# Kernel optimization log

Hardware: AMD Instinct MI355X
Metric: run time of the kernel (lower is better)

Reference implementation:

```python
import jax, jax.numpy as jnp
import numpy as np

L = 2    # num_graph_layers
T = 16   # num_tasks (batch of episodes)
N = 128  # num_samples (nodes per episode)
F = 128  # num_node_feats
BN_EPS = 1e-5


def setup_inputs() -> dict:
    key = jax.random.key(0)
    ks = jax.random.split(key, 8)
    return {
        "node_feats": jax.random.normal(ks[0], (T, N, F), dtype=jnp.float32),
        "edge_feats": jax.random.uniform(ks[1], (T, N, N, F), dtype=jnp.float32),
        # Conv3d(3->1, 1x1x1) weight+bias per layer -> 3 scalars + 1 bias
        "edge_w": (jax.random.normal(ks[2], (L, 3), dtype=jnp.float32) * 0.5),
        "edge_b": (jax.random.normal(ks[3], (L,), dtype=jnp.float32) * 0.1),
        # Conv2d(2->1, 1x1, no bias) -> 2 scalars per layer
        "comb_w": (jax.random.normal(ks[4], (L, 2), dtype=jnp.float32) * 0.5),
        # Conv1d(F->F, k=1, no bias) -> [out,in] per layer
        "node_w": (jax.random.normal(ks[5], (L, F, F), dtype=jnp.float32) / np.sqrt(F).astype(np.float32)),
        # BatchNorm1d affine params
        "bn_gamma": jnp.ones((L, F), dtype=jnp.float32),
        "bn_beta": jnp.zeros((L, F), dtype=jnp.float32),
    }


def _lrelu(x):
    return jnp.where(x >= 0, x, 0.01 * x)  # torch LeakyReLU default slope


def _sim_cal(x):
    # x: [T,N,F] -> clamped [cos_sim, 1-cos_sim]: [T,2,N,N]
    g = jnp.einsum('tnf,tmf->tnm', x, x)
    nrm = jnp.linalg.norm(x, axis=-1)              # [T,N]
    denom = nrm[:, :, None] * nrm[:, None, :] + 1e-6
    sim = (g / denom)[:, None]                     # [T,1,N,N]
    pred = jnp.concatenate([sim, 1.0 - sim], axis=1)
    return jnp.clip(pred, 0.0, 1.0)


def reference(node_feats, edge_feats, edge_w, edge_b, comb_w, node_w, bn_gamma, bn_beta):
    outs = [_sim_cal(node_feats)]
    n = node_feats.shape[1]
    diag_mask = (1.0 - jnp.eye(n, dtype=node_feats.dtype))[None, :, :, None]  # [1,N,N,1]
    for l in range(L):
        x = node_feats                                     # [T,N,F]
        # --- EdgeUpdateNetwork: Conv3d(3->1,1x1x1) over channels [x_i, x_i-x_j, edge] + tanh ---
        diff = x[:, :, None, :] - x[:, None, :, :]         # [T,N,N,F]
        xi = jnp.broadcast_to(x[:, :, None, :], diff.shape)
        e = jnp.tanh(edge_w[l, 0] * xi + edge_w[l, 1] * diff
                     + edge_w[l, 2] * edge_feats + edge_b[l])
        edge_feats = e * diag_mask                         # zero diagonal
        # --- NodeUpdateNetwork ---
        aggr = edge_feats.sum(axis=2)                      # [T,N,F]
        h = _lrelu(comb_w[l, 0] * x + comb_w[l, 1] * aggr) # Conv2d(2->1) + LeakyReLU
        y = jnp.einsum('tnf,gf->tng', h, node_w[l])        # Conv1d(F->F, k=1)
        mu = y.mean(axis=(0, 1))                           # BN over (batch, length)
        var = y.var(axis=(0, 1))
        y = (y - mu) * jax.lax.rsqrt(var + BN_EPS) * bn_gamma[l] + bn_beta[l]
        node_feats = _lrelu(y)
        outs.append(_sim_cal(node_feats))
    return tuple(outs)
```

## Files before the change

kernel.cpp:

```cpp
#include <hip/hip_runtime.h>

#define T_ 16
#define N_ 128
#define F_ 128

__device__ __forceinline__ float fast_tanh(float x) {
    float e = __expf(2.0f * x);
    return 1.0f - __fdividef(2.0f, e + 1.0f);
}

__device__ __forceinline__ float lrelu(float v) {
    return v >= 0.0f ? v : 0.01f * v;
}

__global__ __launch_bounds__(128) void sim_cal_k(const float* __restrict__ x,
                                                 float* __restrict__ out) {
    __shared__ float Xs[128][132];
    __shared__ float nrm[128];
    int t = blockIdx.x, ch = blockIdx.y;
    int m = threadIdx.x;
    const float* xt = x + (size_t)t * (N_ * F_);

    int fg = (m & 31) * 4, ko = m >> 5;
    for (int kb = 0; kb < 128; kb += 4) {
        int k = kb + ko;
        float4 v = *(const float4*)(xt + k * 128 + fg);
        *(float4*)&Xs[k][fg] = v;
    }
    __syncthreads();

    float s = 0.0f;
    #pragma unroll 8
    for (int f = 0; f < 128; f += 4) {
        float4 v = *(float4*)&Xs[m][f];
        s += v.x * v.x + v.y * v.y + v.z * v.z + v.w * v.w;
    }
    nrm[m] = sqrtf(s);
    __syncthreads();

    float acc[16];
    #pragma unroll
    for (int r = 0; r < 16; ++r) acc[r] = 0.0f;

    for (int fc = 0; fc < 128; fc += 32) {
        float xm[32];
        #pragma unroll
        for (int f = 0; f < 32; f += 4) {
            float4 v = *(float4*)&Xs[m][fc + f];
            xm[f] = v.x; xm[f + 1] = v.y; xm[f + 2] = v.z; xm[f + 3] = v.w;
        }
        #pragma unroll
        for (int r = 0; r < 16; ++r) {
            int n = ch * 16 + r;
            #pragma unroll
            for (int f = 0; f < 32; f += 4) {
                float4 v = *(float4*)&Xs[n][fc + f];
                acc[r] = fmaf(xm[f], v.x,
                         fmaf(xm[f + 1], v.y,
                         fmaf(xm[f + 2], v.z,
                         fmaf(xm[f + 3], v.w, acc[r]))));
            }
        }
    }

    float nm = nrm[m];
    size_t ob = (size_t)t * 2 * 16384;
    #pragma unroll
    for (int r = 0; r < 16; ++r) {
        int n = ch * 16 + r;
        float denom = nrm[n] * nm + 1e-6f;
        float sim = __fdividef(acc[r], denom);
        float s0 = fminf(fmaxf(sim, 0.0f), 1.0f);
        float s1 = fminf(fmaxf(1.0f - sim, 0.0f), 1.0f);
        out[ob + (size_t)n * 128 + m] = s0;
        out[ob + 16384 + (size_t)n * 128 + m] = s1;
    }
}

__global__ __launch_bounds__(128) void edge_aggr_l0(const float* __restrict__ x0,
                                                    const float* __restrict__ E,
                                                    const float* __restrict__ ew,
                                                    const float* __restrict__ eb,
                                                    float* __restrict__ aggr) {
    int ti = blockIdx.x;
    int t = ti >> 7, i = ti & 127;
    int tid = threadIdx.x;
    int jl = tid >> 5, fg = tid & 31;
    float w0 = ew[0], w1 = ew[1], w2 = ew[2], b = eb[0];
    const float4* xt = (const float4*)(x0 + (size_t)t * 16384);
    const float4* Ei = (const float4*)(E + (size_t)ti * 16384);
    float4 xi = xt[i * 32 + fg];
    float ax = 0.0f, ay = 0.0f, az = 0.0f, aw = 0.0f;
    #pragma unroll 4
    for (int jb = 0; jb < 128; jb += 4) {
        int j = jb + jl;
        float4 xj = xt[j * 32 + fg];
        float4 ev = Ei[j * 32 + fg];
        if (j != i) {
            ax += fast_tanh(fmaf(w0, xi.x, fmaf(w1, xi.x - xj.x, fmaf(w2, ev.x, b))));
            ay += fast_tanh(fmaf(w0, xi.y, fmaf(w1, xi.y - xj.y, fmaf(w2, ev.y, b))));
            az += fast_tanh(fmaf(w0, xi.z, fmaf(w1, xi.z - xj.z, fmaf(w2, ev.z, b))));
            aw += fast_tanh(fmaf(w0, xi.w, fmaf(w1, xi.w - xj.w, fmaf(w2, ev.w, b))));
        }
    }
    __shared__ float4 red[128];
    red[tid] = make_float4(ax, ay, az, aw);
    __syncthreads();
    if (tid < 32) {
        float4 a = red[tid], b4 = red[tid + 32], c = red[tid + 64], d = red[tid + 96];
        float4 r;
        r.x = a.x + b4.x + c.x + d.x;
        r.y = a.y + b4.y + c.y + d.y;
        r.z = a.z + b4.z + c.z + d.z;
        r.w = a.w + b4.w + c.w + d.w;
        ((float4*)aggr)[(size_t)ti * 32 + tid] = r;
    }
}

__global__ __launch_bounds__(128) void edge_aggr_l1(const float* __restrict__ x0,
                                                    const float* __restrict__ x1,
                                                    const float* __restrict__ E,
                                                    const float* __restrict__ ew,
                                                    const float* __restrict__ eb,
                                                    float* __restrict__ aggr) {
    int ti = blockIdx.x;
    int t = ti >> 7, i = ti & 127;
    int tid = threadIdx.x;
    int jl = tid >> 5, fg = tid & 31;
    float w00 = ew[0], w01 = ew[1], w02 = ew[2], b0 = eb[0];
    float w10 = ew[3], w11 = ew[4], w12 = ew[5], b1 = eb[1];
    const float4* xt0 = (const float4*)(x0 + (size_t)t * 16384);
    const float4* xt1 = (const float4*)(x1 + (size_t)t * 16384);
    const float4* Ei = (const float4*)(E + (size_t)ti * 16384);
    float4 xi0 = xt0[i * 32 + fg];
    float4 xi1 = xt1[i * 32 + fg];
    float ax = 0.0f, ay = 0.0f, az = 0.0f, aw = 0.0f;
    #pragma unroll 2
    for (int jb = 0; jb < 128; jb += 4) {
        int j = jb + jl;
        float4 xj0 = xt0[j * 32 + fg];
        float4 xj1 = xt1[j * 32 + fg];
        float4 ev = Ei[j * 32 + fg];
        if (j != i) {
            float e0x = fast_tanh(fmaf(w00, xi0.x, fmaf(w01, xi0.x - xj0.x, fmaf(w02, ev.x, b0))));
            float e0y = fast_tanh(fmaf(w00, xi0.y, fmaf(w01, xi0.y - xj0.y, fmaf(w02, ev.y, b0))));
            float e0z = fast_tanh(fmaf(w00, xi0.z, fmaf(w01, xi0.z - xj0.z, fmaf(w02, ev.z, b0))));
            float e0w = fast_tanh(fmaf(w00, xi0.w, fmaf(w01, xi0.w - xj0.w, fmaf(w02, ev.w, b0))));
            ax += fast_tanh(fmaf(w10, xi1.x, fmaf(w11, xi1.x - xj1.x, fmaf(w12, e0x, b1))));
            ay += fast_tanh(fmaf(w10, xi1.y, fmaf(w11, xi1.y - xj1.y, fmaf(w12, e0y, b1))));
            az += fast_tanh(fmaf(w10, xi1.z, fmaf(w11, xi1.z - xj1.z, fmaf(w12, e0z, b1))));
            aw += fast_tanh(fmaf(w10, xi1.w, fmaf(w11, xi1.w - xj1.w, fmaf(w12, e0w, b1))));
        }
    }
    __shared__ float4 red[128];
    red[tid] = make_float4(ax, ay, az, aw);
    __syncthreads();
    if (tid < 32) {
        float4 a = red[tid], b4 = red[tid + 32], c = red[tid + 64], d = red[tid + 96];
        float4 r;
        r.x = a.x + b4.x + c.x + d.x;
        r.y = a.y + b4.y + c.y + d.y;
        r.z = a.z + b4.z + c.z + d.z;
        r.w = a.w + b4.w + c.w + d.w;
        ((float4*)aggr)[(size_t)ti * 32 + tid] = r;
    }
}

__global__ void transpose_w(const float* __restrict__ W, float* __restrict__ WT) {
    int l = blockIdx.y;
    int idx = blockIdx.x * 256 + threadIdx.x;
    int g = idx >> 7, f = idx & 127;
    WT[l * 16384 + f * 128 + g] = W[l * 16384 + idx];
}

__global__ void zero_bn(float* __restrict__ bn) {
    bn[threadIdx.x] = 0.0f;
}

#define ROWS 8
__global__ __launch_bounds__(128) void node_update(const float* __restrict__ x,
                                                   float* ag_y,
                                                   const float* __restrict__ cw,
                                                   const float* __restrict__ WT,
                                                   float* __restrict__ bn) {
    __shared__ float hs[ROWS][128];
    int t = blockIdx.x, ch = blockIdx.y, g = threadIdx.x;
    float c0 = cw[0], c1 = cw[1];
    size_t base = ((size_t)t * 128 + ch * ROWS) * 128;
    #pragma unroll
    for (int r = 0; r < ROWS; ++r) {
        float xv = x[base + r * 128 + g];
        float av = ag_y[base + r * 128 + g];
        hs[r][g] = lrelu(fmaf(c0, xv, c1 * av));
    }
    __syncthreads();
    float acc[ROWS];
    #pragma unroll
    for (int r = 0; r < ROWS; ++r) acc[r] = 0.0f;
    #pragma unroll 4
    for (int f2 = 0; f2 < 128; ++f2) {
        float wv = WT[f2 * 128 + g];
        #pragma unroll
        for (int r = 0; r < ROWS; ++r) acc[r] = fmaf(hs[r][f2], wv, acc[r]);
    }
    float s = 0.0f, ss = 0.0f;
    #pragma unroll
    for (int r = 0; r < ROWS; ++r) {
        ag_y[base + r * 128 + g] = acc[r];
        s += acc[r];
        ss += acc[r] * acc[r];
    }
    atomicAdd(&bn[g], s);
    atomicAdd(&bn[128 + g], ss);
}

__global__ void bn_apply(const float* __restrict__ y, const float* __restrict__ bn,
                         const float* __restrict__ gamma, const float* __restrict__ beta,
                         float* __restrict__ xout) {
    int idx = blockIdx.x * 256 + threadIdx.x;
    int g = idx & 127;
    float mu = bn[g] * (1.0f / 2048.0f);
    float var = bn[128 + g] * (1.0f / 2048.0f) - mu * mu;
    float inv = rsqrtf(var + 1e-5f);
    float v = (y[idx] - mu) * inv * gamma[g] + beta[g];
    xout[idx] = lrelu(v);
}

extern "C" void kernel_launch(void* const* d_in, const int* in_sizes, int n_in,
                              void* d_out, int out_size, void* d_ws, size_t ws_size,
                              hipStream_t stream) {
    const float* x0    = (const float*)d_in[0];
    const float* E     = (const float*)d_in[1];
    const float* ew    = (const float*)d_in[2];
    const float* eb    = (const float*)d_in[3];
    const float* cw    = (const float*)d_in[4];
    const float* nw    = (const float*)d_in[5];
    const float* gamma = (const float*)d_in[6];
    const float* beta  = (const float*)d_in[7];
    float* out = (float*)d_out;

    float* ws  = (float*)d_ws;
    float* x1  = ws;
    float* x2  = ws + 262144;
    float* yag = ws + 524288;
    float* bn  = ws + 786432;
    float* WT  = ws + 786688;

    transpose_w<<<dim3(64, 2), 256, 0, stream>>>(nw, WT);

    sim_cal_k<<<dim3(16, 8), 128, 0, stream>>>(x0, out);

    edge_aggr_l0<<<2048, 128, 0, stream>>>(x0, E, ew, eb, yag);
    zero_bn<<<1, 256, 0, stream>>>(bn);
    node_update<<<dim3(16, 16), 128, 0, stream>>>(x0, yag, cw, WT, bn);
    bn_apply<<<1024, 256, 0, stream>>>(yag, bn, gamma, beta, x1);
    sim_cal_k<<<dim3(16, 8), 128, 0, stream>>>(x1, out + 524288);

    edge_aggr_l1<<<2048, 128, 0, stream>>>(x0, x1, E, ew, eb, yag);
    zero_bn<<<1, 256, 0, stream>>>(bn);
    node_update<<<dim3(16, 16), 128, 0, stream>>>(x1, yag, cw + 2, WT + 16384, bn);
    bn_apply<<<1024, 256, 0, stream>>>(yag, bn, gamma + 128, beta + 128, x2);
    sim_cal_k<<<dim3(16, 8), 128, 0, stream>>>(x2, out + 1048576);
}
```

Measured before the change: 343.0 us.

## Fuse edge aggregation with node update and BN apply into sim kernel

Merges edge aggregation, the node-update matvec and the BN statistics accumulation into one per-node kernel with 256 threads. The separate zero_bn and transpose kernels are folded into a single prep kernel, and the BN normalize plus LeakyReLU step moves into the sim_cal load stage, which also writes x1 when needed. The aim is to cut launch count and the intermediate global round-trips. In exchange each block now issues an atomicAdd per feature (2048 blocks contending on 256 addresses) and runs a small serial matvec per node.

```diff
diff --git a/kernel.cpp b/kernel.cpp
--- a/kernel.cpp
+++ b/kernel.cpp
@@ -13,18 +13,62 @@
     return v >= 0.0f ? v : 0.01f * v;
 }
 
-__global__ __launch_bounds__(128) void sim_cal_k(const float* __restrict__ x,
-                                                 float* __restrict__ out) {
+__global__ void wprep(const float* __restrict__ W, float* __restrict__ WT,
+                      float* __restrict__ bn) {
+    int l = blockIdx.y;
+    int idx = blockIdx.x * 256 + threadIdx.x;
+    int g = idx >> 7, f = idx & 127;
+    WT[l * 16384 + f * 128 + g] = W[l * 16384 + idx];
+    if (l == 0 && blockIdx.x == 0) {
+        bn[threadIdx.x] = 0.0f;
+        bn[256 + threadIdx.x] = 0.0f;
+    }
+}
+
+template<bool BN>
+__global__ __launch_bounds__(128) void sim_k(const float* __restrict__ x,
+                                             const float* __restrict__ bnS,
+                                             const float* __restrict__ gamma,
+                                             const float* __restrict__ beta,
+                                             float* __restrict__ out,
+                                             float* __restrict__ xout) {
     __shared__ float Xs[128][132];
     __shared__ float nrm[128];
     int t = blockIdx.x, ch = blockIdx.y;
     int m = threadIdx.x;
     const float* xt = x + (size_t)t * (N_ * F_);
-
     int fg = (m & 31) * 4, ko = m >> 5;
+
+    float4 sc, sh;
+    if constexpr (BN) {
+        float4 s1 = *(const float4*)(bnS + fg);
+        float4 s2 = *(const float4*)(bnS + 128 + fg);
+        float4 ga = *(const float4*)(gamma + fg);
+        float4 be = *(const float4*)(beta + fg);
+        const float inv_n = 1.0f / 2048.0f;
+        float mx = s1.x * inv_n, my = s1.y * inv_n, mz = s1.z * inv_n, mw = s1.w * inv_n;
+        sc.x = rsqrtf(s2.x * inv_n - mx * mx + 1e-5f) * ga.x;
+        sc.y = rsqrtf(s2.y * inv_n - my * my + 1e-5f) * ga.y;
+        sc.z = rsqrtf(s2.z * inv_n - mz * mz + 1e-5f) * ga.z;
+        sc.w = rsqrtf(s2.w * inv_n - mw * mw + 1e-5f) * ga.w;
+        sh.x = be.x - mx * sc.x;
+        sh.y = be.y - my * sc.y;
+        sh.z = be.z - mz * sc.z;
+        sh.w = be.w - mw * sc.w;
+    }
+
+    bool wout = false;
+    if constexpr (BN) wout = (ch == 0) && (xout != nullptr);
     for (int kb = 0; kb < 128; kb += 4) {
         int k = kb + ko;
         float4 v = *(const float4*)(xt + k * 128 + fg);
+        if constexpr (BN) {
+            v.x = lrelu(fmaf(v.x, sc.x, sh.x));
+            v.y = lrelu(fmaf(v.y, sc.y, sh.y));
+            v.z = lrelu(fmaf(v.z, sc.z, sh.z));
+            v.w = lrelu(fmaf(v.w, sc.w, sh.w));
+            if (wout) *(float4*)(xout + (size_t)t * 16384 + k * 128 + fg) = v;
+        }
         *(float4*)&Xs[k][fg] = v;
     }
     __syncthreads();
@@ -77,153 +121,106 @@
     }
 }
 
-__global__ __launch_bounds__(128) void edge_aggr_l0(const float* __restrict__ x0,
-                                                    const float* __restrict__ E,
-                                                    const float* __restrict__ ew,
-                                                    const float* __restrict__ eb,
-                                                    float* __restrict__ aggr) {
+template<int LAYER>
+__global__ __launch_bounds__(256) void layer_fused(const float* __restrict__ x0,
+                                                   const float* __restrict__ x1,
+                                                   const float* __restrict__ E,
+                                                   const float* __restrict__ ew,
+                                                   const float* __restrict__ eb,
+                                                   const float* __restrict__ cw,
+                                                   const float* __restrict__ WT,
+                                                   float* __restrict__ y_out,
+                                                   float* __restrict__ bnL) {
+    __shared__ float4 red[256];
+    __shared__ __align__(16) float aggr[128];
+    __shared__ float hs[128];
+    __shared__ float yred[128];
+
     int ti = blockIdx.x;
     int t = ti >> 7, i = ti & 127;
     int tid = threadIdx.x;
     int jl = tid >> 5, fg = tid & 31;
-    float w0 = ew[0], w1 = ew[1], w2 = ew[2], b = eb[0];
-    const float4* xt = (const float4*)(x0 + (size_t)t * 16384);
-    const float4* Ei = (const float4*)(E + (size_t)ti * 16384);
-    float4 xi = xt[i * 32 + fg];
-    float ax = 0.0f, ay = 0.0f, az = 0.0f, aw = 0.0f;
-    #pragma unroll 4
-    for (int jb = 0; jb < 128; jb += 4) {
-        int j = jb + jl;
-        float4 xj = xt[j * 32 + fg];
-        float4 ev = Ei[j * 32 + fg];
-        if (j != i) {
-            ax += fast_tanh(fmaf(w0, xi.x, fmaf(w1, xi.x - xj.x, fmaf(w2, ev.x, b))));
-            ay += fast_tanh(fmaf(w0, xi.y, fmaf(w1, xi.y - xj.y, fmaf(w2, ev.y, b))));
-            az += fast_tanh(fmaf(w0, xi.z, fmaf(w1, xi.z - xj.z, fmaf(w2, ev.z, b))));
-            aw += fast_tanh(fmaf(w0, xi.w, fmaf(w1, xi.w - xj.w, fmaf(w2, ev.w, b))));
-        }
-    }
-    __shared__ float4 red[128];
-    red[tid] = make_float4(ax, ay, az, aw);
-    __syncthreads();
-    if (tid < 32) {
-        float4 a = red[tid], b4 = red[tid + 32], c = red[tid + 64], d = red[tid + 96];
-        float4 r;
-        r.x = a.x + b4.x + c.x + d.x;
-        r.y = a.y + b4.y + c.y + d.y;
-        r.z = a.z + b4.z + c.z + d.z;
-        r.w = a.w + b4.w + c.w + d.w;
-        ((float4*)aggr)[(size_t)ti * 32 + tid] = r;
-    }
-}
-
-__global__ __launch_bounds__(128) void edge_aggr_l1(const float* __restrict__ x0,
-                                                    const float* __restrict__ x1,
-                                                    const float* __restrict__ E,
-                                                    const float* __restrict__ ew,
-                                                    const float* __restrict__ eb,
-                                                    float* __restrict__ aggr) {
-    int ti = blockIdx.x;
-    int t = ti >> 7, i = ti & 127;
-    int tid = threadIdx.x;
-    int jl = tid >> 5, fg = tid & 31;
-    float w00 = ew[0], w01 = ew[1], w02 = ew[2], b0 = eb[0];
-    float w10 = ew[3], w11 = ew[4], w12 = ew[5], b1 = eb[1];
+
     const float4* xt0 = (const float4*)(x0 + (size_t)t * 16384);
     const float4* xt1 = (const float4*)(x1 + (size_t)t * 16384);
-    const float4* Ei = (const float4*)(E + (size_t)ti * 16384);
+    const float4* Ei  = (const float4*)(E + (size_t)ti * 16384);
+
+    float w00 = ew[0], w01 = ew[1], w02 = ew[2], b0 = eb[0];
+    float w10 = 0.f, w11 = 0.f, w12 = 0.f, b1 = 0.f;
+    if constexpr (LAYER == 1) { w10 = ew[3]; w11 = ew[4]; w12 = ew[5]; b1 = eb[1]; }
+
     float4 xi0 = xt0[i * 32 + fg];
-    float4 xi1 = xt1[i * 32 + fg];
-    float ax = 0.0f, ay = 0.0f, az = 0.0f, aw = 0.0f;
-    #pragma unroll 2
-    for (int jb = 0; jb < 128; jb += 4) {
-        int j = jb + jl;
-        float4 xj0 = xt0[j * 32 + fg];
-        float4 xj1 = xt1[j * 32 + fg];
-        float4 ev = Ei[j * 32 + fg];
-        if (j != i) {
-            float e0x = fast_tanh(fmaf(w00, xi0.x, fmaf(w01, xi0.x - xj0.x, fmaf(w02, ev.x, b0))));
-            float e0y = fast_tanh(fmaf(w00, xi0.y, fmaf(w01, xi0.y - xj0.y, fmaf(w02, ev.y, b0))));
-            float e0z = fast_tanh(fmaf(w00, xi0.z, fmaf(w01, xi0.z - xj0.z, fmaf(w02, ev.z, b0))));
-            float e0w = fast_tanh(fmaf(w00, xi0.w, fmaf(w01, xi0.w - xj0.w, fmaf(w02, ev.w, b0))));
-            ax += fast_tanh(fmaf(w10, xi1.x, fmaf(w11, xi1.x - xj1.x, fmaf(w12, e0x, b1))));
-            ay += fast_tanh(fmaf(w10, xi1.y, fmaf(w11, xi1.y - xj1.y, fmaf(w12, e0y, b1))));
-            az += fast_tanh(fmaf(w10, xi1.z, fmaf(w11, xi1.z - xj1.z, fmaf(w12, e0z, b1))));
-            aw += fast_tanh(fmaf(w10, xi1.w, fmaf(w11, xi1.w - xj1.w, fmaf(w12, e0w, b1))));
-        }
-    }
-    __shared__ float4 red[128];
+    float4 xi1 = xi0;
+    if constexpr (LAYER == 1) xi1 = xt1[i * 32 + fg];
+
+    float ax = 0.f, ay = 0.f, az = 0.f, aw = 0.f;
+    if constexpr (LAYER == 0) {
+        #pragma unroll 4
+        for (int jb = 0; jb < 128; jb += 8) {
+            int j = jb + jl;
+            float4 ev  = Ei[j * 32 + fg];
+            float4 xj0 = xt0[j * 32 + fg];
+            if (j != i) {
+                ax += fast_tanh(fmaf(w00, xi0.x, fmaf(w01, xi0.x - xj0.x, fmaf(w02, ev.x, b0))));
+                ay += fast_tanh(fmaf(w00, xi0.y, fmaf(w01, xi0.y - xj0.y, fmaf(w02, ev.y, b0))));
+                az += fast_tanh(fmaf(w00, xi0.z, fmaf(w01, xi0.z - xj0.z, fmaf(w02, ev.z, b0))));
+                aw += fast_tanh(fmaf(w00, xi0.w, fmaf(w01, xi0.w - xj0.w, fmaf(w02, ev.w, b0))));
+            }
+        }
+    } else {
+        #pragma unroll 2
+        for (int jb = 0; jb < 128; jb += 8) {
+            int j = jb + jl;
+            float4 ev  = Ei[j * 32 + fg];
+            float4 xj0 = xt0[j * 32 + fg];
+            float4 xj1 = xt1[j * 32 + fg];
+            if (j != i) {
+                float e0x = fast_tanh(fmaf(w00, xi0.x, fmaf(w01, xi0.x - xj0.x, fmaf(w02, ev.x, b0))));
+                float e0y = fast_tanh(fmaf(w00, xi0.y, fmaf(w01, xi0.y - xj0.y, fmaf(w02, ev.y, b0))));
+                float e0z = fast_tanh(fmaf(w00, xi0.z, fmaf(w01, xi0.z - xj0.z, fmaf(w02, ev.z, b0))));
+                float e0w = fast_tanh(fmaf(w00, xi0.w, fmaf(w01, xi0.w - xj0.w, fmaf(w02, ev.w, b0))));
+                ax += fast_tanh(fmaf(w10, xi1.x, fmaf(w11, xi1.x - xj1.x, fmaf(w12, e0x, b1))));
+                ay += fast_tanh(fmaf(w10, xi1.y, fmaf(w11, xi1.y - xj1.y, fmaf(w12, e0y, b1))));
+                az += fast_tanh(fmaf(w10, xi1.z, fmaf(w11, xi1.z - xj1.z, fmaf(w12, e0z, b1))));
+                aw += fast_tanh(fmaf(w10, xi1.w, fmaf(w11, xi1.w - xj1.w, fmaf(w12, e0w, b1))));
+            }
+        }
+    }
+
     red[tid] = make_float4(ax, ay, az, aw);
     __syncthreads();
     if (tid < 32) {
-        float4 a = red[tid], b4 = red[tid + 32], c = red[tid + 64], d = red[tid + 96];
-        float4 r;
-        r.x = a.x + b4.x + c.x + d.x;
-        r.y = a.y + b4.y + c.y + d.y;
-        r.z = a.z + b4.z + c.z + d.z;
-        r.w = a.w + b4.w + c.w + d.w;
-        ((float4*)aggr)[(size_t)ti * 32 + tid] = r;
-    }
-}
-
-__global__ void transpose_w(const float* __restrict__ W, float* __restrict__ WT) {
-    int l = blockIdx.y;
-    int idx = blockIdx.x * 256 + threadIdx.x;
-    int g = idx >> 7, f = idx & 127;
-    WT[l * 16384 + f * 128 + g] = W[l * 16384 + idx];
-}
-
-__global__ void zero_bn(float* __restrict__ bn) {
-    bn[threadIdx.x] = 0.0f;
-}
-
-#define ROWS 8
-__global__ __launch_bounds__(128) void node_update(const float* __restrict__ x,
-                                                   float* ag_y,
-                                                   const float* __restrict__ cw,
-                                                   const float* __restrict__ WT,
-                                                   float* __restrict__ bn) {
-    __shared__ float hs[ROWS][128];
-    int t = blockIdx.x, ch = blockIdx.y, g = threadIdx.x;
-    float c0 = cw[0], c1 = cw[1];
-    size_t base = ((size_t)t * 128 + ch * ROWS) * 128;
-    #pragma unroll
-    for (int r = 0; r < ROWS; ++r) {
-        float xv = x[base + r * 128 + g];
-        float av = ag_y[base + r * 128 + g];
-        hs[r][g] = lrelu(fmaf(c0, xv, c1 * av));
-    }
-    __syncthreads();
-    float acc[ROWS];
-    #pragma unroll
-    for (int r = 0; r < ROWS; ++r) acc[r] = 0.0f;
-    #pragma unroll 4
-    for (int f2 = 0; f2 < 128; ++f2) {
-        float wv = WT[f2 * 128 + g];
+        float4 r = red[tid];
         #pragma unroll
-        for (int r = 0; r < ROWS; ++r) acc[r] = fmaf(hs[r][f2], wv, acc[r]);
-    }
-    float s = 0.0f, ss = 0.0f;
-    #pragma unroll
-    for (int r = 0; r < ROWS; ++r) {
-        ag_y[base + r * 128 + g] = acc[r];
-        s += acc[r];
-        ss += acc[r] * acc[r];
-    }
-    atomicAdd(&bn[g], s);
-    atomicAdd(&bn[128 + g], ss);
-}
-
-__global__ void bn_apply(const float* __restrict__ y, const float* __restrict__ bn,
-                         const float* __restrict__ gamma, const float* __restrict__ beta,
-                         float* __restrict__ xout) {
-    int idx = blockIdx.x * 256 + threadIdx.x;
-    int g = idx & 127;
-    float mu = bn[g] * (1.0f / 2048.0f);
-    float var = bn[128 + g] * (1.0f / 2048.0f) - mu * mu;
-    float inv = rsqrtf(var + 1e-5f);
-    float v = (y[idx] - mu) * inv * gamma[g] + beta[g];
-    xout[idx] = lrelu(v);
+        for (int k = 1; k < 8; ++k) {
+            float4 o = red[tid + 32 * k];
+            r.x += o.x; r.y += o.y; r.z += o.z; r.w += o.w;
+        }
+        ((float4*)aggr)[tid] = r;
+    }
+    __syncthreads();
+
+    if (tid < 128) {
+        const float* xin = (LAYER == 0) ? x0 : x1;
+        float xv = xin[(size_t)t * 16384 + (size_t)i * 128 + tid];
+        hs[tid] = lrelu(fmaf(cw[0], xv, cw[1] * aggr[tid]));
+    }
+    __syncthreads();
+
+    int g = tid & 127, half = tid >> 7;
+    float acc = 0.f;
+    const float* wp = WT + (size_t)(half * 64) * 128 + g;
+    const float* hp = hs + half * 64;
+    #pragma unroll 8
+    for (int f = 0; f < 64; ++f) acc = fmaf(hp[f], wp[(size_t)f * 128], acc);
+    if (half) yred[g] = acc;
+    __syncthreads();
+    if (!half) {
+        float y = acc + yred[g];
+        y_out[(size_t)ti * 128 + g] = y;
+        atomicAdd(&bnL[g], y);
+        atomicAdd(&bnL[128 + g], y * y);
+    }
 }
 
 extern "C" void kernel_launch(void* const* d_in, const int* in_sizes, int n_in,
@@ -241,24 +238,18 @@
 
     float* ws  = (float*)d_ws;
     float* x1  = ws;
-    float* x2  = ws + 262144;
-    float* yag = ws + 524288;
-    float* bn  = ws + 786432;
-    float* WT  = ws + 786688;
-
-    transpose_w<<<dim3(64, 2), 256, 0, stream>>>(nw, WT);
-
-    sim_cal_k<<<dim3(16, 8), 128, 0, stream>>>(x0, out);
-
-    edge_aggr_l0<<<2048, 128, 0, stream>>>(x0, E, ew, eb, yag);
-    zero_bn<<<1, 256, 0, stream>>>(bn);
-    node_update<<<dim3(16, 16), 128, 0, stream>>>(x0, yag, cw, WT, bn);
-    bn_apply<<<1024, 256, 0, stream>>>(yag, bn, gamma, beta, x1);
-    sim_cal_k<<<dim3(16, 8), 128, 0, stream>>>(x1, out + 524288);
-
-    edge_aggr_l1<<<2048, 128, 0, stream>>>(x0, x1, E, ew, eb, yag);
-    zero_bn<<<1, 256, 0, stream>>>(bn);
-    node_update<<<dim3(16, 16), 128, 0, stream>>>(x1, yag, cw + 2, WT + 16384, bn);
-    bn_apply<<<1024, 256, 0, stream>>>(yag, bn, gamma + 128, beta + 128, x2);
-    sim_cal_k<<<dim3(16, 8), 128, 0, stream>>>(x2, out + 1048576);
-}
+    float* yag = ws + 262144;
+    float* bn  = ws + 524288;
+    float* WT  = ws + 524800;
+
+    wprep<<<dim3(64, 2), 256, 0, stream>>>(nw, WT, bn);
+
+    sim_k<false><<<dim3(16, 8), 128, 0, stream>>>(x0, nullptr, nullptr, nullptr, out, nullptr);
+
+    layer_fused<0><<<2048, 256, 0, stream>>>(x0, x0, E, ew, eb, cw, WT, yag, bn);
+    sim_k<true><<<dim3(16, 8), 128, 0, stream>>>(yag, bn, gamma, beta, out + 524288, x1);
+
+    layer_fused<1><<<2048, 256, 0, stream>>>(x0, x1, E, ew, eb, cw + 2, WT + 16384, yag, bn + 256);
+    sim_k<true><<<dim3(16, 8), 128, 0, stream>>>(yag, bn + 256, gamma + 128, beta + 128,
+                                                 out + 1048576, nullptr);
+}
```

Measured after the change: 384.7 us. +12.1%, slower.
